# Kernel tuning notes

Measured on AMD Instinct MI355X. Metric: run time of the kernel, lower is better.

## Reference

```python
import jax, jax.numpy as jnp
import numpy as np

B, D_MODEL, H, W = 4, 128, 128, 128
HEAD_DIM = 16
GROUP = D_MODEL // HEAD_DIM          # 8 deformable groups
D_INNER = D_MODEL                    # expand = 1
D_STATE = 1
DT_RANK = 8                          # ceil(d_model / 16)
D_CONV = 3
EPS = 1e-6


def setup_inputs() -> dict:
    key = jax.random.key(0)
    ks = jax.random.split(key, 10)
    f = jnp.float32
    # dt bias init as in DASSM.dt_init (dt in [1e-3, 1e-1], inverse-softplus)
    dt = jnp.exp(jax.random.uniform(ks[7], (D_INNER,), f)
                 * (np.log(0.1) - np.log(0.001)) + np.log(0.001))
    dt = jnp.clip(dt, 1e-4)
    dt_b = dt + jnp.log(-jnp.expm1(-dt))
    s = DT_RANK ** -0.5
    return dict(
        x=jax.random.normal(ks[0], (B, D_MODEL, H, W), f),
        in_proj_w=jax.random.normal(ks[1], (D_INNER, D_MODEL), f) * (D_MODEL ** -0.5),
        conv2d_w=jax.random.normal(ks[2], (D_INNER, 1, D_CONV, D_CONV), f) * 0.1,
        conv2d_b=jnp.zeros((D_INNER,), f),
        dw_w=jax.random.normal(ks[3], (D_INNER, 1, 3, 3), f) * 0.1,
        dw_b=jnp.zeros((D_INNER,), f),
        dw_ln_g=jnp.ones((D_INNER,), f),
        dw_ln_b=jnp.zeros((D_INNER,), f),
        off_w=jax.random.normal(ks[4], (GROUP * 2, D_INNER), f) * 0.01,
        off_b=jnp.zeros((GROUP * 2,), f),
        x_proj_w=jax.random.normal(ks[5], (DT_RANK + 2 * D_STATE, D_INNER), f) * (D_INNER ** -0.5),
        dt_w=jax.random.uniform(ks[6], (D_INNER, DT_RANK), f, -s, s),
        dt_b=dt_b,
        A_logs=jnp.tile(jnp.log(jnp.arange(1, D_STATE + 1, dtype=f))[None, :], (D_INNER, 1)),
        Ds=jnp.ones((D_INNER,), f),
        out_ln_g=jnp.ones((D_INNER,), f),
        out_ln_b=jnp.zeros((D_INNER,), f),
        out_proj_w=jax.random.normal(ks[8], (D_MODEL, D_INNER), f) * (D_INNER ** -0.5),
    )


def _layer_norm(x, g, b):
    m = x.mean(-1, keepdims=True)
    v = ((x - m) ** 2).mean(-1, keepdims=True)
    return (x - m) * jax.lax.rsqrt(v + EPS) * g + b


def _dwconv(x, w, b):
    # x: (B,C,H,W), w: (C,1,k,k) depthwise, 'SAME' == torch padding=(k-1)//2
    out = jax.lax.conv_general_dilated(
        x, w, (1, 1), 'SAME', feature_group_count=x.shape[1],
        dimension_numbers=('NCHW', 'OIHW', 'NCHW'))
    return out + b[None, :, None, None]


def _dcn_sample(img_last, offset):
    # DCNv3 with kernel_size=1, mask=1: sampling point = pixel center + offset.
    # img_last: (B,H,W,C); offset: (B,H,W,G*2) laid out (x,y) per group.
    b, h, w, c = img_last.shape
    gc = c // GROUP
    img = img_last.reshape(b, h, w, GROUP, gc)
    off = offset.reshape(b, h, w, GROUP, 2)
    px = jnp.arange(w, dtype=offset.dtype)[None, None, :, None] + off[..., 0]
    py = jnp.arange(h, dtype=offset.dtype)[None, :, None, None] + off[..., 1]
    y0 = jnp.floor(py)
    x0 = jnp.floor(px)
    wy = py - y0
    wx = px - x0
    bi = jnp.arange(b)[:, None, None, None]
    gi = jnp.arange(GROUP)[None, None, None, :]

    def tap(yi, xi, wgt):  # zero-padding bilinear tap (grid_sample, align_corners=False)
        valid = (yi >= 0) & (yi < h) & (xi >= 0) & (xi < w)
        yc = jnp.clip(yi, 0, h - 1).astype(jnp.int32)
        xc = jnp.clip(xi, 0, w - 1).astype(jnp.int32)
        v = img[bi, yc, xc, gi]  # (B,H,W,G,gc)
        return v * (wgt * valid)[..., None]

    out = (tap(y0, x0, (1 - wy) * (1 - wx)) + tap(y0, x0 + 1, (1 - wy) * wx)
           + tap(y0 + 1, x0, wy * (1 - wx)) + tap(y0 + 1, x0 + 1, wy * wx))
    return out.reshape(b, h, w, c)


def _selective_scan(xs, dts, A, Bs, Cs, Ds, dt_bias):
    # xs,dts: (B,D,L); A: (D,N); Bs,Cs: (B,N,L); delta_softplus=True
    delta = jax.nn.softplus(dts + dt_bias[None, :, None])
    dA = jnp.exp(jnp.einsum('bdl,dn->lbdn', delta, A))          # (L,B,D,N)
    dBx = jnp.einsum('bdl,bnl,bdl->lbdn', delta, Bs, xs)          # (L,B,D,N)
    C_t = jnp.transpose(Cs, (2, 0, 1))                            # (L,B,N)

    def step(hc, inputs):
        dA_t, dBx_t, c = inputs
        hc = dA_t * hc + dBx_t
        return hc, jnp.einsum('bdn,bn->bd', hc, c)

    h0 = jnp.zeros(dA.shape[1:], xs.dtype)
    _, ys = jax.lax.scan(step, h0, (dA, dBx, C_t))                # ys: (L,B,D)
    y = jnp.transpose(ys, (1, 2, 0))                              # (B,D,L)
    return y + Ds[None, :, None] * xs


def reference(x, in_proj_w, conv2d_w, conv2d_b, dw_w, dw_b, dw_ln_g, dw_ln_b,
              off_w, off_b, x_proj_w, dt_w, dt_b, A_logs, Ds,
              out_ln_g, out_ln_b, out_proj_w):
    # in_proj (1x1 conv, no bias) then depthwise conv + SiLU
    xin = jnp.einsum('bchw,oc->bohw', x, in_proj_w)
    xc = jax.nn.silu(_dwconv(xin, conv2d_w, conv2d_b))
    # Dynamic_Adaptive_Scan: dwconv -> LN(channels_last) -> GELU -> offsets -> DCNv3(k=1)
    x1 = _dwconv(xc, dw_w, dw_b)
    x1 = jax.nn.gelu(_layer_norm(jnp.transpose(x1, (0, 2, 3, 1)), dw_ln_g, dw_ln_b),
                     approximate=False)
    offset = x1 @ off_w.T + off_b                                  # (B,H,W,G*2)
    xd = _dcn_sample(jnp.transpose(xc, (0, 2, 3, 1)), offset)      # (B,H,W,C)
    xd = jnp.transpose(xd, (0, 3, 1, 2))                           # (B,C,H,W)
    # SSM (Mamba selective scan over L = H*W)
    Bn, C, Hh, Ww = xd.shape
    L = Hh * Ww
    xs = xd.reshape(Bn, C, L)
    x_dbl = jnp.einsum('rc,bcl->brl', x_proj_w, xs)
    dts, Bs, Cs = jnp.split(x_dbl, [DT_RANK, DT_RANK + D_STATE], axis=1)
    dts = jnp.einsum('dr,brl->bdl', dt_w, dts)
    A = -jnp.exp(A_logs)
    y = _selective_scan(xs, dts, A, Bs, Cs, Ds, dt_b).reshape(Bn, C, Hh, Ww)
    # out LayerNorm (over channels) + out_proj (1x1, no bias)
    y = jnp.transpose(_layer_norm(jnp.transpose(y, (0, 2, 3, 1)), out_ln_g, out_ln_b),
                      (0, 3, 1, 2))
    return jnp.einsum('bchw,oc->bohw', y, out_proj_w)
```

## Files before the change

### kernel.cpp

```cpp
#include <hip/hip_runtime.h>
#include <hip/hip_bf16.h>

typedef unsigned short u16;
typedef unsigned int u32;
typedef __bf16 bf16x8 __attribute__((ext_vector_type(8)));
typedef float f32x4 __attribute__((ext_vector_type(4)));

__device__ __forceinline__ float bfu(u16 u) { return __uint_as_float(((u32)u) << 16); }
__device__ __forceinline__ u16 fbf(float f) {
  __hip_bfloat16 h = __float2bfloat16(f);
  return *reinterpret_cast<u16*>(&h);
}
__device__ __forceinline__ float softplusf(float z) {
  float t = __expf(z);
  return (z > 20.f) ? z : __logf(1.f + t);
}
__device__ __forceinline__ float lo16(u32 p) { return __uint_as_float(p << 16); }
__device__ __forceinline__ float hi16(u32 p) { return __uint_as_float(p & 0xffff0000u); }
__device__ __forceinline__ bf16x8 ld_bf8(const u16* p) {
  union { uint4 u; bf16x8 v; } c;
  c.u = *(const uint4*)p;
  return c.v;
}

__global__ __launch_bounds__(256) void k_inproj(const float* __restrict__ X,
                                                const float* __restrict__ W,
                                                u16* __restrict__ out,
                                                const float* __restrict__ W2,
                                                const float* __restrict__ gO,
                                                const float* __restrict__ bO,
                                                float* __restrict__ s12) {
  __shared__ __align__(16) u16 Ws[128 * 136];
  __shared__ __align__(16) u16 Xs[64 * 136];
  int tid = threadIdx.x;
  if (blockIdx.x == 1024) {
    if (tid < 128) {
      int o = tid;
      float s1 = 0.f, s2 = 0.f;
      for (int c = 0; c < 128; ++c) {
        float w = W2[(o << 7) + c];
        s1 = fmaf(w, bO[c], s1);
        s2 = fmaf(w, gO[c], s2);
      }
      s12[o] = s1;
      s12[128 + o] = s2;
    }
    return;
  }
  int b = blockIdx.x >> 8;
  int l0 = (blockIdx.x & 255) << 6;
  for (int i = 0; i < 16; ++i) {
    int idx = (i << 8) + tid;
    int o = idx >> 5, c4 = (idx & 31) << 2;
    float4 w4 = *(const float4*)&W[(o << 7) + c4];
    ushort4 s;
    s.x = fbf(w4.x); s.y = fbf(w4.y); s.z = fbf(w4.z); s.w = fbf(w4.w);
    *(ushort4*)&Ws[o * 136 + c4] = s;
  }
  for (int i = 0; i < 8; ++i) {
    int idx = (i << 8) + tid;
    int c = idx >> 4, lq = (idx & 15) << 2;
    float4 x4 = *(const float4*)&X[(((long)(b << 7) + c) << 14) + l0 + lq];
    Xs[(lq + 0) * 136 + c] = fbf(x4.x);
    Xs[(lq + 1) * 136 + c] = fbf(x4.y);
    Xs[(lq + 2) * 136 + c] = fbf(x4.z);
    Xs[(lq + 3) * 136 + c] = fbf(x4.w);
  }
  __syncthreads();
  int w = tid >> 6, lane = tid & 63;
  int mrow = lane & 15, quad = lane >> 4;
  f32x4 acc[2][4];
#pragma unroll
  for (int ot = 0; ot < 2; ++ot)
#pragma unroll
    for (int lt = 0; lt < 4; ++lt) acc[ot][lt] = (f32x4){0.f, 0.f, 0.f, 0.f};
#pragma unroll
  for (int kb = 0; kb < 4; ++kb) {
    int c0 = (kb << 5) + (quad << 3);
    bf16x8 af[2], bfr[4];
#pragma unroll
    for (int ot = 0; ot < 2; ++ot)
      af[ot] = ld_bf8(&Ws[((w << 5) + (ot << 4) + mrow) * 136 + c0]);
#pragma unroll
    for (int lt = 0; lt < 4; ++lt)
      bfr[lt] = ld_bf8(&Xs[((lt << 4) + mrow) * 136 + c0]);
#pragma unroll
    for (int ot = 0; ot < 2; ++ot)
#pragma unroll
      for (int lt = 0; lt < 4; ++lt)
        acc[ot][lt] = __builtin_amdgcn_mfma_f32_16x16x32_bf16(af[ot], bfr[lt], acc[ot][lt], 0, 0, 0);
  }
#pragma unroll
  for (int ot = 0; ot < 2; ++ot)
#pragma unroll
    for (int lt = 0; lt < 4; ++lt) {
      int l = l0 + (lt << 4) + mrow;
      int o = (w << 5) + (ot << 4) + (quad << 2);
      ushort4 s;
      s.x = fbf(acc[ot][lt][0]); s.y = fbf(acc[ot][lt][1]);
      s.z = fbf(acc[ot][lt][2]); s.w = fbf(acc[ot][lt][3]);
      *(ushort4*)&out[(((long)(b << 14) + l) << 7) + o] = s;
    }
}

__global__ __launch_bounds__(256) void k_dwconv(const u16* __restrict__ in,
                                                const float* __restrict__ w9,
                                                const float* __restrict__ bias,
                                                u16* __restrict__ out) {
  __shared__ float wsT[9][128];
  __shared__ float bs[128];
  int tid = threadIdx.x;
  for (int i = 0; i < 5; ++i) {
    int lin = (i << 8) + tid;
    if (lin < 1152) { int c = lin / 9, k = lin - 9 * c; wsT[k][c] = w9[lin]; }
  }
  if (tid < 128) bs[tid] = bias[tid];
  __syncthreads();
  int blk = blockIdx.x;
  int b = blk >> 10;
  int s = blk & 1023;
  int h = s >> 3;
  int w = ((s & 7) << 4) + (tid >> 4);
  int c0 = (tid & 15) << 3;
  const u16* bbase = in + ((long)b << 21);
  float acc[8];
  {
    float4 b0 = *(const float4*)&bs[c0];
    float4 b1 = *(const float4*)&bs[c0 + 4];
    acc[0] = b0.x; acc[1] = b0.y; acc[2] = b0.z; acc[3] = b0.w;
    acc[4] = b1.x; acc[5] = b1.y; acc[6] = b1.z; acc[7] = b1.w;
  }
#pragma unroll
  for (int ky = -1; ky <= 1; ++ky) {
    int y = h + ky;
    if ((unsigned)y >= 128u) continue;
#pragma unroll
    for (int kx = -1; kx <= 1; ++kx) {
      int x = w + kx;
      if ((unsigned)x >= 128u) continue;
      int k = (ky + 1) * 3 + (kx + 1);
      uint4 v = *(const uint4*)(bbase + ((((y << 7) + x)) << 7) + c0);
      float4 w0 = *(const float4*)&wsT[k][c0];
      float4 w1 = *(const float4*)&wsT[k][c0 + 4];
      u32 vv[4] = {v.x, v.y, v.z, v.w};
      float wf[8] = {w0.x, w0.y, w0.z, w0.w, w1.x, w1.y, w1.z, w1.w};
#pragma unroll
      for (int cc = 0; cc < 8; ++cc) {
        float xv = (cc & 1) ? hi16(vv[cc >> 1]) : lo16(vv[cc >> 1]);
        acc[cc] = fmaf(wf[cc], xv, acc[cc]);
      }
    }
  }
#pragma unroll
  for (int cc = 0; cc < 8; ++cc) acc[cc] = acc[cc] / (1.f + __expf(-acc[cc]));
  ushort4 s0, s1;
  s0.x = fbf(acc[0]); s0.y = fbf(acc[1]); s0.z = fbf(acc[2]); s0.w = fbf(acc[3]);
  s1.x = fbf(acc[4]); s1.y = fbf(acc[5]); s1.z = fbf(acc[6]); s1.w = fbf(acc[7]);
  u16* po = out + ((long)b << 21) + ((((h << 7) + w)) << 7) + c0;
  *(ushort4*)po = s0;
  *(ushort4*)(po + 4) = s1;
}

__global__ __launch_bounds__(256) void k_dwoff(const u16* __restrict__ in,
                                               const float* __restrict__ w9,
                                               const float* __restrict__ bias,
                                               const float* __restrict__ g,
                                               const float* __restrict__ bt,
                                               const float* __restrict__ offw,
                                               const float* __restrict__ offb,
                                               float* __restrict__ offs) {
  __shared__ float wsT[9][128];
  __shared__ float bs[128], gs[128], bsh[128];
  __shared__ __align__(16) u16 Ge[16 * 136];
  __shared__ __align__(16) u16 Wos[16 * 136];
  int tid = threadIdx.x;
  for (int i = 0; i < 5; ++i) {
    int lin = (i << 8) + tid;
    if (lin < 1152) { int c = lin / 9, k = lin - 9 * c; wsT[k][c] = w9[lin]; }
  }
  if (tid < 128) { bs[tid] = bias[tid]; gs[tid] = g[tid]; bsh[tid] = bt[tid]; }
  for (int i = 0; i < 8; ++i) {
    int idx = (i << 8) + tid;
    int o = idx >> 7, c = idx & 127;
    Wos[o * 136 + c] = fbf(offw[idx]);
  }
  __syncthreads();
  int blk = blockIdx.x;
  int b = blk >> 10;
  int s = blk & 1023;
  int h = s >> 3;
  int p = tid >> 4;
  int w = ((s & 7) << 4) + p;
  int c0 = (tid & 15) << 3;
  const u16* bbase = in + ((long)b << 21);
  float acc[8];
  {
    float4 b0 = *(const float4*)&bs[c0];
    float4 b1 = *(const float4*)&bs[c0 + 4];
    acc[0] = b0.x; acc[1] = b0.y; acc[2] = b0.z; acc[3] = b0.w;
    acc[4] = b1.x; acc[5] = b1.y; acc[6] = b1.z; acc[7] = b1.w;
  }
#pragma unroll
  for (int ky = -1; ky <= 1; ++ky) {
    int y = h + ky;
    if ((unsigned)y >= 128u) continue;
#pragma unroll
    for (int kx = -1; kx <= 1; ++kx) {
      int x = w + kx;
      if ((unsigned)x >= 128u) continue;
      int k = (ky + 1) * 3 + (kx + 1);
      uint4 v = *(const uint4*)(bbase + ((((y << 7) + x)) << 7) + c0);
      float4 w0 = *(const float4*)&wsT[k][c0];
      float4 w1 = *(const float4*)&wsT[k][c0 + 4];
      u32 vv[4] = {v.x, v.y, v.z, v.w};
      float wf[8] = {w0.x, w0.y, w0.z, w0.w, w1.x, w1.y, w1.z, w1.w};
#pragma unroll
      for (int cc = 0; cc < 8; ++cc) {
        float xv = (cc & 1) ? hi16(vv[cc >> 1]) : lo16(vv[cc >> 1]);
        acc[cc] = fmaf(wf[cc], xv, acc[cc]);
      }
    }
  }
  float sum = 0.f, ssum = 0.f;
#pragma unroll
  for (int cc = 0; cc < 8; ++cc) { sum += acc[cc]; ssum = fmaf(acc[cc], acc[cc], ssum); }
#pragma unroll
  for (int off = 1; off < 16; off <<= 1) {
    sum += __shfl_xor(sum, off);
    ssum += __shfl_xor(ssum, off);
  }
  float m = sum * (1.f / 128.f);
  float r = rsqrtf(ssum * (1.f / 128.f) - m * m + 1e-6f);
  {
    u32 pk[4];
#pragma unroll
    for (int jj = 0; jj < 4; ++jj) {
      u16 h2[2];
#pragma unroll
      for (int e = 0; e < 2; ++e) {
        int cc = 2 * jj + e;
        float xn = fmaf((acc[cc] - m) * r, gs[c0 + cc], bsh[c0 + cc]);
        h2[e] = fbf(0.5f * xn * (1.f + erff(xn * 0.70710678118f)));
      }
      pk[jj] = (u32)h2[0] | ((u32)h2[1] << 16);
    }
    *(uint4*)&Ge[p * 136 + c0] = make_uint4(pk[0], pk[1], pk[2], pk[3]);
  }
  __syncthreads();
  if (tid < 64) {
    int lane = tid;
    int mrow = lane & 15, quad = lane >> 4;
    f32x4 acc0 = (f32x4){0.f, 0.f, 0.f, 0.f};
#pragma unroll
    for (int kb = 0; kb < 4; ++kb) {
      int cb = (kb << 5) + (quad << 3);
      bf16x8 af = ld_bf8(&Wos[mrow * 136 + cb]);
      bf16x8 bfr = ld_bf8(&Ge[mrow * 136 + cb]);
      acc0 = __builtin_amdgcn_mfma_f32_16x16x32_bf16(af, bfr, acc0, 0, 0, 0);
    }
    int l = (h << 7) + ((s & 7) << 4) + mrow;
    float2* po = (float2*)offs;
    int o0 = quad << 2;
    po[(((long)((b << 3) + (quad << 1))) << 14) + l] =
        make_float2(acc0[0] + offb[o0], acc0[1] + offb[o0 + 1]);
    po[(((long)((b << 3) + (quad << 1) + 1)) << 14) + l] =
        make_float2(acc0[2] + offb[o0 + 2], acc0[3] + offb[o0 + 3]);
  }
}

__global__ __launch_bounds__(512, 8) void k_dcn(const u16* __restrict__ xc,
                                                const float* __restrict__ offs,
                                                const float* __restrict__ xpw,
                                                const float* __restrict__ dtw,
                                                u16* __restrict__ xs,
                                                u16* __restrict__ dts,
                                                float* __restrict__ Bsb,
                                                float* __restrict__ Csb) {
  __shared__ __align__(16) u16 xds_bf[64 * 132];
  __shared__ __align__(16) float xdblT[8 * 64];
  __shared__ __align__(16) float xpwS[10 * 8 * 20];
  int tid = threadIdx.x;
  for (int i = 0; i < 3; ++i) {
    int idx = (i << 9) + tid;
    if (idx < 1280) {
      int rr = idx >> 7, rem = idx & 127;
      xpwS[((rr << 3) + (rem >> 4)) * 20 + (rem & 15)] = xpw[idx];
    }
  }
  int blk = blockIdx.x;
  int b = blk >> 8;
  int l0 = (blk & 255) << 6;
  int gg = tid & 7, p = tid >> 3;
  int l = l0 + p, hh = l >> 7, ww = l & 127;
  float2 off = ((const float2*)offs)[(((long)((b << 3) + gg)) << 14) + l];
  float px = (float)ww + off.x, py = (float)hh + off.y;
  float x0f = floorf(px), y0f = floorf(py);
  float wx = px - x0f, wy = py - y0f;
  int ix = (int)x0f, iy = (int)y0f;
  float acc[16];
#pragma unroll
  for (int ch = 0; ch < 16; ++ch) acc[ch] = 0.f;
  const u16* bbase = xc + ((long)b << 21) + (gg << 4);
  int xi[4] = {ix, ix + 1, ix, ix + 1};
  int yi[4] = {iy, iy, iy + 1, iy + 1};
  float wt4[4] = {(1.f - wy) * (1.f - wx), (1.f - wy) * wx, wy * (1.f - wx), wy * wx};
#pragma unroll
  for (int t = 0; t < 4; ++t) {
    if (wt4[t] != 0.f && (unsigned)yi[t] < 128u && (unsigned)xi[t] < 128u) {
      const u16* pp = bbase + ((((yi[t] << 7) + xi[t])) << 7);
      uint4 v0 = *(const uint4*)pp;
      uint4 v1 = *(const uint4*)(pp + 8);
      float wv = wt4[t];
      u32 vv[8] = {v0.x, v0.y, v0.z, v0.w, v1.x, v1.y, v1.z, v1.w};
#pragma unroll
      for (int ch = 0; ch < 16; ++ch) {
        float xv = (ch & 1) ? hi16(vv[ch >> 1]) : lo16(vv[ch >> 1]);
        acc[ch] = fmaf(wv, xv, acc[ch]);
      }
    }
  }
  {
    u32 pk[8];
#pragma unroll
    for (int j = 0; j < 8; ++j)
      pk[j] = (u32)fbf(acc[2 * j]) | ((u32)fbf(acc[2 * j + 1]) << 16);
    u16* row = &xds_bf[p * 132 + (gg << 4)];
#pragma unroll
    for (int q = 0; q < 4; ++q)
      *(uint2*)(row + (q << 2)) = make_uint2(pk[2 * q], pk[2 * q + 1]);
  }
  __syncthreads();
  {
    float pr[10];
#pragma unroll
    for (int rr = 0; rr < 10; ++rr) {
      const float* wr = &xpwS[((rr << 3) + gg) * 20];
      float4 w0 = *(const float4*)wr;
      float4 w1 = *(const float4*)(wr + 4);
      float4 w2 = *(const float4*)(wr + 8);
      float4 w3 = *(const float4*)(wr + 12);
      float sv = 0.f;
      sv = fmaf(w0.x, acc[0], sv);  sv = fmaf(w0.y, acc[1], sv);
      sv = fmaf(w0.z, acc[2], sv);  sv = fmaf(w0.w, acc[3], sv);
      sv = fmaf(w1.x, acc[4], sv);  sv = fmaf(w1.y, acc[5], sv);
      sv = fmaf(w1.z, acc[6], sv);  sv = fmaf(w1.w, acc[7], sv);
      sv = fmaf(w2.x, acc[8], sv);  sv = fmaf(w2.y, acc[9], sv);
      sv = fmaf(w2.z, acc[10], sv); sv = fmaf(w2.w, acc[11], sv);
      sv = fmaf(w3.x, acc[12], sv); sv = fmaf(w3.y, acc[13], sv);
      sv = fmaf(w3.z, acc[14], sv); sv = fmaf(w3.w, acc[15], sv);
      pr[rr] = sv;
    }
#pragma unroll
    for (int rr = 0; rr < 10; ++rr) {
      float v = pr[rr];
      v += __shfl_xor(v, 1);
      v += __shfl_xor(v, 2);
      v += __shfl_xor(v, 4);
      pr[rr] = v;
    }
    if (gg == 0) {
#pragma unroll
      for (int rr = 0; rr < 8; ++rr) xdblT[(rr << 6) + p] = pr[rr];
      Bsb[((long)b << 14) + l0 + p] = pr[8];
      Csb[((long)b << 14) + l0 + p] = pr[9];
    }
  }
  __syncthreads();
#pragma unroll
  for (int it = 0; it < 2; ++it) {
    int task = (it << 9) + tid;
    int cc = task >> 3, t = task & 7;
    u32 pk[4];
#pragma unroll
    for (int jj = 0; jj < 4; ++jj) {
      u16 a0 = xds_bf[((t << 3) + 2 * jj + 0) * 132 + cc];
      u16 a1 = xds_bf[((t << 3) + 2 * jj + 1) * 132 + cc];
      pk[jj] = (u32)a0 | ((u32)a1 << 16);
    }
    *(uint4*)&xs[(((long)(b << 7) + cc) << 14) + l0 + (t << 3)] =
        make_uint4(pk[0], pk[1], pk[2], pk[3]);
  }
  {
    int dd = tid >> 3, t = tid & 7;
    float4 a0 = *(const float4*)&dtw[dd << 3];
    float4 a1 = *(const float4*)&dtw[(dd << 3) + 4];
    float4 b0 = *(const float4*)&dtw[(dd + 64) << 3];
    float4 b1 = *(const float4*)&dtw[((dd + 64) << 3) + 4];
    float wr0[8] = {a0.x, a0.y, a0.z, a0.w, a1.x, a1.y, a1.z, a1.w};
    float wr1[8] = {b0.x, b0.y, b0.z, b0.w, b1.x, b1.y, b1.z, b1.w};
    float y0[8], y1[8];
#pragma unroll
    for (int j = 0; j < 8; ++j) { y0[j] = 0.f; y1[j] = 0.f; }
#pragma unroll
    for (int rr = 0; rr < 8; ++rr) {
      float w0 = wr0[rr], w1 = wr1[rr];
      const float* xr = &xdblT[(rr << 6) + (t << 3)];
      float4 xa = *(const float4*)xr;
      float4 xb = *(const float4*)(xr + 4);
      float xv[8] = {xa.x, xa.y, xa.z, xa.w, xb.x, xb.y, xb.z, xb.w};
#pragma unroll
      for (int j = 0; j < 8; ++j) {
        y0[j] = fmaf(w0, xv[j], y0[j]);
        y1[j] = fmaf(w1, xv[j], y1[j]);
      }
    }
    u32 pk0[4], pk1[4];
#pragma unroll
    for (int jj = 0; jj < 4; ++jj) {
      pk0[jj] = (u32)fbf(y0[2 * jj]) | ((u32)fbf(y0[2 * jj + 1]) << 16);
      pk1[jj] = (u32)fbf(y1[2 * jj]) | ((u32)fbf(y1[2 * jj + 1]) << 16);
    }
    *(uint4*)&dts[(((long)(b << 7) + dd) << 14) + l0 + (t << 3)] =
        make_uint4(pk0[0], pk0[1], pk0[2], pk0[3]);
    *(uint4*)&dts[(((long)(b << 7) + dd + 64) << 14) + l0 + (t << 3)] =
        make_uint4(pk1[0], pk1[1], pk1[2], pk1[3]);
  }
}

__global__ __launch_bounds__(1024) void k_scan(u16* __restrict__ xy,
                                               const u16* __restrict__ dts16,
                                               const float* __restrict__ Bsb,
                                               const float* __restrict__ Csb,
                                               const float* __restrict__ A_logs,
                                               const float* __restrict__ Dsv,
                                               const float* __restrict__ dtbv) {
  __shared__ float swp[16], swe[16];
  int bd = blockIdx.x;
  int b = bd >> 7, d = bd & 127;
  float Ad = -__expf(A_logs[d]);
  float dtb = dtbv[d];
  float Dd = Dsv[d];
  int t = threadIdx.x;
  int lane = t & 63, wid = t >> 6;
  long base = ((long)bd << 14) + (t << 4);
  long bb = ((long)b << 14) + (t << 4);
  const uint4* pz4 = (const uint4*)(dts16 + base);
  const uint4* px4 = (const uint4*)(xy + base);
  const float4* pB = (const float4*)(Bsb + bb);
  const float4* pC = (const float4*)(Csb + bb);
  uint4 zA = pz4[0], zB = pz4[1];
  uint4 xA = px4[0], xB = px4[1];
  u32 zw[8] = {zA.x, zA.y, zA.z, zA.w, zB.x, zB.y, zB.z, zB.w};
  u32 xw[8] = {xA.x, xA.y, xA.z, xA.w, xB.x, xB.y, xB.z, xB.w};
  float E = 0.f, P = 1.f;
#pragma unroll
  for (int q = 0; q < 4; ++q) {
    float4 B4 = pB[q];
    float Bq[4] = {B4.x, B4.y, B4.z, B4.w};
#pragma unroll
    for (int j = 0; j < 4; ++j) {
      int k = (q << 2) + j;
      float z = (k & 1) ? hi16(zw[k >> 1]) : lo16(zw[k >> 1]);
      float xv = (k & 1) ? hi16(xw[k >> 1]) : lo16(xw[k >> 1]);
      float delta = softplusf(z + dtb);
      float a = __expf(delta * Ad);
      E = fmaf(a, E, delta * Bq[j] * xv);
      P *= a;
    }
  }
#pragma unroll
  for (int off = 1; off < 64; off <<= 1) {
    float Pp = __shfl_up(P, off);
    float Ep = __shfl_up(E, off);
    if (lane >= off) { E = fmaf(P, Ep, E); P *= Pp; }
  }
  if (lane == 63) { swp[wid] = P; swe[wid] = E; }
  __syncthreads();
  if (t < 16) {
    float p2 = swp[t], e2 = swe[t];
#pragma unroll
    for (int off = 1; off < 16; off <<= 1) {
      float pp = __shfl_up(p2, off);
      float ee = __shfl_up(e2, off);
      if (t >= off) { e2 = fmaf(p2, ee, e2); p2 *= pp; }
    }
    swp[t] = p2; swe[t] = e2;
  }
  __syncthreads();
  float hw = (wid == 0) ? 0.f : swe[wid - 1];
  float Pex = __shfl_up(P, 1);
  float Eex = __shfl_up(E, 1);
  if (lane == 0) { Pex = 1.f; Eex = 0.f; }
  float h = fmaf(Pex, hw, Eex);
  u32 ypk[8];
#pragma unroll
  for (int q = 0; q < 4; ++q) {
    float4 B4 = pB[q];
    float4 C4 = pC[q];
    float Bq[4] = {B4.x, B4.y, B4.z, B4.w};
    float Cq[4] = {C4.x, C4.y, C4.z, C4.w};
#pragma unroll
    for (int j = 0; j < 4; ++j) {
      int k = (q << 2) + j;
      float z = (k & 1) ? hi16(zw[k >> 1]) : lo16(zw[k >> 1]);
      float xv = (k & 1) ? hi16(xw[k >> 1]) : lo16(xw[k >> 1]);
      float delta = softplusf(z + dtb);
      float a = __expf(delta * Ad);
      h = fmaf(a, h, delta * Bq[j] * xv);
      u16 yb = fbf(fmaf(Dd, xv, h * Cq[j]));
      if ((k & 1) == 0) ypk[k >> 1] = yb; else ypk[k >> 1] |= (u32)yb << 16;
    }
  }
  uint4* py = (uint4*)(xy + base);
  py[0] = make_uint4(ypk[0], ypk[1], ypk[2], ypk[3]);
  py[1] = make_uint4(ypk[4], ypk[5], ypk[6], ypk[7]);
}

__global__ __launch_bounds__(256) void k_outproj(const u16* __restrict__ y,
                                                 const float* __restrict__ W2,
                                                 const float* __restrict__ g,
                                                 const float* __restrict__ s12,
                                                 float* __restrict__ out) {
  __shared__ __align__(16) u16 Ws[128 * 136];
  __shared__ __align__(16) u16 Ys[64 * 136];
  __shared__ float ps[4][64], pss[4][64];
  __shared__ float mean_s[64], rstd_s[64];
  int tid = threadIdx.x;
  int b = blockIdx.x >> 8;
  int l0 = (blockIdx.x & 255) << 6;
  for (int i = 0; i < 16; ++i) {
    int idx = (i << 8) + tid;
    int o = idx >> 5, c4 = (idx & 31) << 2;
    float4 w4 = *(const float4*)&W2[(o << 7) + c4];
    ushort4 s;
    s.x = fbf(w4.x * g[c4]);     s.y = fbf(w4.y * g[c4 + 1]);
    s.z = fbf(w4.z * g[c4 + 2]); s.w = fbf(w4.w * g[c4 + 3]);
    *(ushort4*)&Ws[o * 136 + c4] = s;
  }
  for (int i = 0; i < 4; ++i) {
    int idx = (i << 8) + tid;
    int c = idx >> 3, lq = (idx & 7) << 3;
    uint4 v = *(const uint4*)&y[(((long)(b << 7) + c) << 14) + l0 + lq];
    u32 vv[4] = {v.x, v.y, v.z, v.w};
#pragma unroll
    for (int r = 0; r < 8; ++r)
      Ys[(lq + r) * 136 + c] = (u16)((r & 1) ? (vv[r >> 1] >> 16) : (vv[r >> 1] & 0xffffu));
  }
  __syncthreads();
  {
    int l = tid & 63, q = tid >> 6;
    const u16* row = &Ys[l * 136 + (q << 5)];
    float s = 0.f, ss = 0.f;
#pragma unroll 8
    for (int c = 0; c < 32; ++c) { float v = bfu(row[c]); s += v; ss = fmaf(v, v, ss); }
    ps[q][l] = s; pss[q][l] = ss;
  }
  __syncthreads();
  if (tid < 64) {
    float s = ps[0][tid] + ps[1][tid] + ps[2][tid] + ps[3][tid];
    float ss = pss[0][tid] + pss[1][tid] + pss[2][tid] + pss[3][tid];
    float m = s * (1.f / 128.f);
    mean_s[tid] = m;
    rstd_s[tid] = rsqrtf(ss * (1.f / 128.f) - m * m + 1e-6f);
  }
  __syncthreads();
  int w = tid >> 6, lane = tid & 63;
  int mrow = lane & 15, quad = lane >> 4;
  f32x4 acc[2][4];
#pragma unroll
  for (int ot = 0; ot < 2; ++ot)
#pragma unroll
    for (int lt = 0; lt < 4; ++lt) acc[ot][lt] = (f32x4){0.f, 0.f, 0.f, 0.f};
#pragma unroll
  for (int kb = 0; kb < 4; ++kb) {
    int c0 = (kb << 5) + (quad << 3);
    bf16x8 af[2], bfr[4];
#pragma unroll
    for (int ot = 0; ot < 2; ++ot)
      af[ot] = ld_bf8(&Ws[((w << 5) + (ot << 4) + mrow) * 136 + c0]);
#pragma unroll
    for (int lt = 0; lt < 4; ++lt)
      bfr[lt] = ld_bf8(&Ys[((lt << 4) + mrow) * 136 + c0]);
#pragma unroll
    for (int ot = 0; ot < 2; ++ot)
#pragma unroll
      for (int lt = 0; lt < 4; ++lt)
        acc[ot][lt] = __builtin_amdgcn_mfma_f32_16x16x32_bf16(af[ot], bfr[lt], acc[ot][lt], 0, 0, 0);
  }
  float s1r[2][4], s2r[2][4];
#pragma unroll
  for (int ot = 0; ot < 2; ++ot)
#pragma unroll
    for (int r = 0; r < 4; ++r) {
      int o = (w << 5) + (ot << 4) + (quad << 2) + r;
      s1r[ot][r] = s12[o];
      s2r[ot][r] = s12[128 + o];
    }
#pragma unroll
  for (int ot = 0; ot < 2; ++ot)
#pragma unroll
    for (int lt = 0; lt < 4; ++lt) {
      int lcol = (lt << 4) + mrow;
      float mv = mean_s[lcol], rv = rstd_s[lcol];
      int obase = (w << 5) + (ot << 4) + (quad << 2);
#pragma unroll
      for (int r = 0; r < 4; ++r) {
        float v = fmaf(rv, acc[ot][lt][r] - mv * s2r[ot][r], s1r[ot][r]);
        out[(((long)(b << 7) + obase + r) << 14) + l0 + lcol] = v;
      }
    }
}

extern "C" void kernel_launch(void* const* d_in, const int* in_sizes, int n_in,
                              void* d_out, int out_size, void* d_ws, size_t ws_size,
                              hipStream_t stream) {
  const float* x         = (const float*)d_in[0];
  const float* in_proj_w = (const float*)d_in[1];
  const float* conv2d_w  = (const float*)d_in[2];
  const float* conv2d_b  = (const float*)d_in[3];
  const float* dw_w      = (const float*)d_in[4];
  const float* dw_b      = (const float*)d_in[5];
  const float* dw_ln_g   = (const float*)d_in[6];
  const float* dw_ln_b   = (const float*)d_in[7];
  const float* off_w     = (const float*)d_in[8];
  const float* off_b     = (const float*)d_in[9];
  const float* x_proj_w  = (const float*)d_in[10];
  const float* dt_w      = (const float*)d_in[11];
  const float* dt_b      = (const float*)d_in[12];
  const float* A_logs    = (const float*)d_in[13];
  const float* Ds        = (const float*)d_in[14];
  const float* out_ln_g  = (const float*)d_in[15];
  const float* out_ln_b  = (const float*)d_in[16];
  const float* out_proj_w= (const float*)d_in[17];
  float* out = (float*)d_out;

  u16* A  = (u16*)d_ws;
  u16* Bx = A + 8388608;
  u16* Dd = Bx + 8388608;
  float* offs  = (float*)(Dd + 8388608);
  float* Bsb   = offs + 1048576;
  float* Csb   = Bsb + 65536;
  float* s12   = Csb + 65536;

  hipLaunchKernelGGL(k_inproj, dim3(1025), dim3(256), 0, stream, x, in_proj_w, A,
                     out_proj_w, out_ln_g, out_ln_b, s12);
  hipLaunchKernelGGL(k_dwconv, dim3(4096), dim3(256), 0, stream, A, conv2d_w, conv2d_b, Bx);
  hipLaunchKernelGGL(k_dwoff, dim3(4096), dim3(256), 0, stream, Bx, dw_w, dw_b,
                     dw_ln_g, dw_ln_b, off_w, off_b, offs);
  hipLaunchKernelGGL(k_dcn, dim3(1024), dim3(512), 0, stream, Bx, offs, x_proj_w, dt_w, A, Dd, Bsb, Csb);
  hipLaunchKernelGGL(k_scan, dim3(512), dim3(1024), 0, stream, A, Dd, Bsb, Csb, A_logs, Ds, dt_b);
  hipLaunchKernelGGL(k_outproj, dim3(1024), dim3(256), 0, stream, A, out_proj_w, out_ln_g, s12, out);
}
```

Baseline: 224.5 us.

## Remap DCN thread layout, use wave-uniform scalar weights and LDS partial-sum reduction

```diff
diff --git a/kernel.cpp b/kernel.cpp
--- a/kernel.cpp
+++ b/kernel.cpp
@@ -277,46 +277,48 @@
                                                 float* __restrict__ Bsb,
                                                 float* __restrict__ Csb) {
   __shared__ __align__(16) u16 xds_bf[64 * 132];
+  __shared__ float part[64 * 81];
   __shared__ __align__(16) float xdblT[8 * 64];
-  __shared__ __align__(16) float xpwS[10 * 8 * 20];
   int tid = threadIdx.x;
-  for (int i = 0; i < 3; ++i) {
-    int idx = (i << 9) + tid;
-    if (idx < 1280) {
-      int rr = idx >> 7, rem = idx & 127;
-      xpwS[((rr << 3) + (rem >> 4)) * 20 + (rem & 15)] = xpw[idx];
-    }
-  }
   int blk = blockIdx.x;
   int b = blk >> 8;
   int l0 = (blk & 255) << 6;
-  int gg = tid & 7, p = tid >> 3;
+  int p = tid & 63, gg = tid >> 6;
   int l = l0 + p, hh = l >> 7, ww = l & 127;
   float2 off = ((const float2*)offs)[(((long)((b << 3) + gg)) << 14) + l];
   float px = (float)ww + off.x, py = (float)hh + off.y;
   float x0f = floorf(px), y0f = floorf(py);
   float wx = px - x0f, wy = py - y0f;
   int ix = (int)x0f, iy = (int)y0f;
+  int x0c = min(max(ix, 0), 127), x1c = min(max(ix + 1, 0), 127);
+  int y0c = min(max(iy, 0), 127), y1c = min(max(iy + 1, 0), 127);
+  float vx0 = ((unsigned)ix < 128u) ? 1.f : 0.f;
+  float vx1 = ((unsigned)(ix + 1) < 128u) ? 1.f : 0.f;
+  float vy0 = ((unsigned)iy < 128u) ? 1.f : 0.f;
+  float vy1 = ((unsigned)(iy + 1) < 128u) ? 1.f : 0.f;
+  float wt4[4] = {(1.f - wy) * (1.f - wx) * vy0 * vx0,
+                  (1.f - wy) * wx * vy0 * vx1,
+                  wy * (1.f - wx) * vy1 * vx0,
+                  wy * wx * vy1 * vx1};
+  const u16* bbase = xc + ((long)b << 21) + (gg << 4);
+  const u16* tp[4];
+  tp[0] = bbase + ((((y0c << 7) + x0c)) << 7);
+  tp[1] = bbase + ((((y0c << 7) + x1c)) << 7);
+  tp[2] = bbase + ((((y1c << 7) + x0c)) << 7);
+  tp[3] = bbase + ((((y1c << 7) + x1c)) << 7);
   float acc[16];
 #pragma unroll
   for (int ch = 0; ch < 16; ++ch) acc[ch] = 0.f;
-  const u16* bbase = xc + ((long)b << 21) + (gg << 4);
-  int xi[4] = {ix, ix + 1, ix, ix + 1};
-  int yi[4] = {iy, iy, iy + 1, iy + 1};
-  float wt4[4] = {(1.f - wy) * (1.f - wx), (1.f - wy) * wx, wy * (1.f - wx), wy * wx};
 #pragma unroll
   for (int t = 0; t < 4; ++t) {
-    if (wt4[t] != 0.f && (unsigned)yi[t] < 128u && (unsigned)xi[t] < 128u) {
-      const u16* pp = bbase + ((((yi[t] << 7) + xi[t])) << 7);
-      uint4 v0 = *(const uint4*)pp;
-      uint4 v1 = *(const uint4*)(pp + 8);
-      float wv = wt4[t];
-      u32 vv[8] = {v0.x, v0.y, v0.z, v0.w, v1.x, v1.y, v1.z, v1.w};
-#pragma unroll
-      for (int ch = 0; ch < 16; ++ch) {
-        float xv = (ch & 1) ? hi16(vv[ch >> 1]) : lo16(vv[ch >> 1]);
-        acc[ch] = fmaf(wv, xv, acc[ch]);
-      }
+    uint4 v0 = *(const uint4*)tp[t];
+    uint4 v1 = *(const uint4*)(tp[t] + 8);
+    float wv = wt4[t];
+    u32 vv[8] = {v0.x, v0.y, v0.z, v0.w, v1.x, v1.y, v1.z, v1.w};
+#pragma unroll
+    for (int ch = 0; ch < 16; ++ch) {
+      float xv = (ch & 1) ? hi16(vv[ch >> 1]) : lo16(vv[ch >> 1]);
+      acc[ch] = fmaf(wv, xv, acc[ch]);
     }
   }
   {
@@ -329,43 +331,34 @@
     for (int q = 0; q < 4; ++q)
       *(uint2*)(row + (q << 2)) = make_uint2(pk[2 * q], pk[2 * q + 1]);
   }
-  __syncthreads();
-  {
-    float pr[10];
-#pragma unroll
-    for (int rr = 0; rr < 10; ++rr) {
-      const float* wr = &xpwS[((rr << 3) + gg) * 20];
-      float4 w0 = *(const float4*)wr;
-      float4 w1 = *(const float4*)(wr + 4);
-      float4 w2 = *(const float4*)(wr + 8);
-      float4 w3 = *(const float4*)(wr + 12);
-      float sv = 0.f;
-      sv = fmaf(w0.x, acc[0], sv);  sv = fmaf(w0.y, acc[1], sv);
-      sv = fmaf(w0.z, acc[2], sv);  sv = fmaf(w0.w, acc[3], sv);
-      sv = fmaf(w1.x, acc[4], sv);  sv = fmaf(w1.y, acc[5], sv);
-      sv = fmaf(w1.z, acc[6], sv);  sv = fmaf(w1.w, acc[7], sv);
-      sv = fmaf(w2.x, acc[8], sv);  sv = fmaf(w2.y, acc[9], sv);
-      sv = fmaf(w2.z, acc[10], sv); sv = fmaf(w2.w, acc[11], sv);
-      sv = fmaf(w3.x, acc[12], sv); sv = fmaf(w3.y, acc[13], sv);
-      sv = fmaf(w3.z, acc[14], sv); sv = fmaf(w3.w, acc[15], sv);
-      pr[rr] = sv;
-    }
-#pragma unroll
-    for (int rr = 0; rr < 10; ++rr) {
-      float v = pr[rr];
-      v += __shfl_xor(v, 1);
-      v += __shfl_xor(v, 2);
-      v += __shfl_xor(v, 4);
-      pr[rr] = v;
-    }
-    if (gg == 0) {
-#pragma unroll
-      for (int rr = 0; rr < 8; ++rr) xdblT[(rr << 6) + p] = pr[rr];
-      Bsb[((long)b << 14) + l0 + p] = pr[8];
-      Csb[((long)b << 14) + l0 + p] = pr[9];
-    }
-  }
-  __syncthreads();
+  {
+    int ggu = __builtin_amdgcn_readfirstlane(gg);
+    const float* wb = xpw + (ggu << 4);
+    int pbase = p * 81 + gg;
+#pragma unroll
+    for (int r = 0; r < 10; ++r) {
+      const float* wr = wb + (r << 7);
+      float s = 0.f;
+#pragma unroll
+      for (int ch = 0; ch < 16; ++ch) s = fmaf(wr[ch], acc[ch], s);
+      part[pbase + (r << 3)] = s;
+    }
+  }
+  __syncthreads();
+  {
+    int task = tid;
+#pragma unroll
+    for (int pass = 0; pass < 2; ++pass, task += 512) {
+      if (task < 640) {
+        int r = task >> 6, p2 = task & 63;
+        const float* pp = &part[p2 * 81 + (r << 3)];
+        float s = ((pp[0] + pp[1]) + (pp[2] + pp[3])) + ((pp[4] + pp[5]) + (pp[6] + pp[7]));
+        if (r < 8) xdblT[(r << 6) + p2] = s;
+        else if (r == 8) Bsb[((long)b << 14) + l0 + p2] = s;
+        else Csb[((long)b << 14) + l0 + p2] = s;
+      }
+    }
+  }
 #pragma unroll
   for (int it = 0; it < 2; ++it) {
     int task = (it << 9) + tid;
@@ -380,6 +373,7 @@
     *(uint4*)&xs[(((long)(b << 7) + cc) << 14) + l0 + (t << 3)] =
         make_uint4(pk[0], pk[1], pk[2], pk[3]);
   }
+  __syncthreads();
   {
     int dd = tid >> 3, t = tid & 7;
     float4 a0 = *(const float4*)&dtw[dd << 3];
```

Result: no change. 221.5 us (-1.3%).
